# Optimization experiments

Measured on AMD Instinct MI355X. Metric: run time of the kernel, lower is better.

The kernel has to match this reference:

```python
import jax, jax.numpy as jnp
import numpy as np

N = 50000      # nodes
E = 800000     # edges (before self-loops)
F_IN = 128     # args.nsegment
H = 4          # args.nhead
C = 32         # args.dhidden
OUT = 64       # output_dim
G = 64         # number of graphs in batch
NEG = 0.2      # args.negslope (and GATv2 internal leaky-relu slope, PyG default 0.2)


def setup_inputs() -> dict:
    key = jax.random.key(0)
    ks = jax.random.split(key, 8)
    def w(k, i, o):
        return jax.random.normal(k, (i, o), jnp.float32) / np.sqrt(i)
    x = jax.random.normal(ks[0], (N, F_IN), jnp.float32)
    edge_index = jax.random.randint(ks[1], (2, E), 0, N, dtype=jnp.int32)
    batch = jnp.sort(jax.random.randint(ks[2], (N,), 0, G, dtype=jnp.int32))
    d = dict(x=x, edge_index=edge_index, batch=batch)
    # layer dims: (in_dim, heads, out_per_head, concat)
    dims = [(F_IN, H, C, True), (H * C, H, C, True), (H * C, 1, OUT, False)]
    for li, (fi, h, c, concat) in enumerate(dims):
        k1, k2, k3 = jax.random.split(ks[3 + li], 3)
        d[f"Wl{li}"] = w(k1, fi, h * c)
        d[f"Wr{li}"] = w(k2, fi, h * c)
        d[f"att{li}"] = jax.random.normal(k3, (h, c), jnp.float32) / np.sqrt(c)
        d[f"b{li}"] = jnp.zeros((h * c if concat else c,), jnp.float32)
    return d


def _gat_layer(x, src, tgt, Wl, Wr, att, b, concat):
    """GATv2Conv: e_ij = att . leaky_relu(Wl x_j + Wr x_i); softmax over edges into i;
    out_i = sum_j alpha_ij * (Wl x_j). src/tgt include self-loops."""
    n = x.shape[0]
    h, c = att.shape
    xl = (x @ Wl).reshape(n, h, c)                 # source transform [N,h,c]
    xr = (x @ Wr).reshape(n, h, c)                 # target transform [N,h,c]
    g = jax.nn.leaky_relu(xl[src] + xr[tgt], NEG)  # [Etot,h,c]
    score = jnp.einsum('ehc,hc->eh', g, att)       # [Etot,h]
    smax = jax.ops.segment_max(score, tgt, num_segments=n)
    ex = jnp.exp(score - smax[tgt])
    den = jax.ops.segment_sum(ex, tgt, num_segments=n)
    alpha = ex / den[tgt]                          # per-target softmax [Etot,h]
    out = jax.ops.segment_sum(xl[src] * alpha[:, :, None], tgt, num_segments=n)
    out = out.reshape(n, h * c) if concat else out.mean(axis=1)
    return out + b


def _forward(x, edge_index, batch, params):
    n = x.shape[0]
    loops = jnp.arange(n, dtype=edge_index.dtype)  # PyG add_self_loops=True
    src = jnp.concatenate([edge_index[0], loops])
    tgt = jnp.concatenate([edge_index[1], loops])
    for Wl, Wr, att, b, concat in params:
        x = _gat_layer(x, src, tgt, Wl, Wr, att, b, concat)
        x = jax.nn.leaky_relu(x, NEG)  # dropout p is identity in eval mode
    ssum = jax.ops.segment_sum(x, batch, num_segments=G)
    cnt = jax.ops.segment_sum(jnp.ones((n,), x.dtype), batch, num_segments=G)
    return ssum / jnp.maximum(cnt, 1.0)[:, None]   # global_mean_pool -> [G, OUT]


def reference(x, edge_index, batch, Wl0, Wr0, att0, b0, Wl1, Wr1, att1, b1, Wl2, Wr2, att2, b2):
    params = [(Wl0, Wr0, att0, b0, True),
              (Wl1, Wr1, att1, b1, True),
              (Wl2, Wr2, att2, b2, False)]
    return _forward(x, edge_index, batch, params)
```

## Files before the change

### kernel.cpp

```cpp
#include <hip/hip_runtime.h>
#include <hip/hip_fp16.h>
#include <math.h>

#define NEGSLOPE 0.2f

typedef _Float16 f16x8 __attribute__((ext_vector_type(8)));
typedef _Float16 f16x2 __attribute__((ext_vector_type(2)));
typedef float f32x4 __attribute__((ext_vector_type(4)));

__device__ __forceinline__ float lrelu(float x) { return x > 0.f ? x : NEGSLOPE * x; }

__device__ __forceinline__ float dot2acc(f16x2 a, f16x2 b, float c) {
#if __has_builtin(__builtin_amdgcn_fdot2)
    return __builtin_amdgcn_fdot2(a, b, c, false);
#else
    return c + (float)a[0] * (float)b[0] + (float)a[1] * (float)b[1];
#endif
}

__global__ __launch_bounds__(256) void k_prep(
        const float* W0, const float* W1, const float* W2,
        const float* W3, const float* W4, const float* W5,
        _Float16* D0, _Float16* D1, _Float16* D2,
        _Float16* D3, _Float16* D4, _Float16* D5,
        int* __restrict__ zbase, int nzero) {
    int b = blockIdx.x, t = threadIdx.x;
    if (b < 320) {
        const float* Ws[6] = {W0, W1, W2, W3, W4, W5};
        _Float16* Ds[6] = {D0, D1, D2, D3, D4, D5};
        int j = b * 256 + t;
        int m, jj, kout;
        if (j < 65536) { m = j >> 14; jj = j & 16383; kout = 128; }
        else           { m = 4 + ((j - 65536) >> 13); jj = (j - 65536) & 8191; kout = 64; }
        int col = jj >> 7, k = jj & 127;
        Ds[m][col * 128 + k] = (_Float16)Ws[m][k * kout + col];
    } else {
        int i = (b - 320) * 256 + t;
        if (i < nzero) zbase[i] = 0;
    }
}

__global__ void k_count(const int* __restrict__ tgt, int* __restrict__ deg,
                        int* __restrict__ rank, int e) {
    int i = blockIdx.x * 256 + threadIdx.x;
    if (i < e) rank[i] = atomicAdd(&deg[tgt[i]], 1);
}
__global__ __launch_bounds__(256) void k_scanA(const int* __restrict__ deg, int* __restrict__ rowptr,
                                               int* __restrict__ bsums, int* __restrict__ bhist, int n) {
    __shared__ int s[256];
    __shared__ int lh[64];
    int t = threadIdx.x;
    if (t < 64) lh[t] = 0;
    int base = blockIdx.x * 4096 + t * 16;
    int pre[16];
    int sum = 0;
    __syncthreads();
    for (int i = 0; i < 16; ++i) {
        int idx = base + i;
        int v = 0;
        if (idx < n) {
            v = deg[idx] + 1;
            atomicAdd(&lh[v < 63 ? v : 63], 1);
        }
        pre[i] = sum;
        sum += v;
    }
    s[t] = sum;
    __syncthreads();
    for (int off = 1; off < 256; off <<= 1) {
        int v = (t >= off) ? s[t - off] : 0;
        __syncthreads();
        s[t] += v;
        __syncthreads();
    }
    int tbase = s[t] - sum;
    for (int i = 0; i < 16; ++i) {
        int idx = base + i;
        if (idx < n) rowptr[idx] = tbase + pre[i];
    }
    if (t == 0) bsums[blockIdx.x] = s[255];
    if (t < 64) bhist[blockIdx.x * 64 + t] = lh[t];
}
__global__ __launch_bounds__(256) void k_scanC(int* __restrict__ rowptr, const int* __restrict__ bsums,
                                               int* __restrict__ edst, const int* __restrict__ deg,
                                               const int* __restrict__ bhist, int* __restrict__ perm,
                                               int nscan, int n) {
    __shared__ int pref[17];
    __shared__ int cur[64];
    __shared__ int bbase[64];
    int t = threadIdx.x;
    if (t == 0) {
        int run = 0;
        for (int k = 0; k < nscan; ++k) { pref[k] = run; run += bsums[k]; }
        pref[nscan] = run;
    }
    if (t < 64) {
        int part = 0, tot = 0;
        for (int sb = 0; sb < nscan; ++sb) {
            int v = bhist[sb * 64 + t];
            if (sb < (int)blockIdx.x) part += v;
            tot += v;
        }
        bbase[t] = tot;
        cur[t] = part;
    }
    __syncthreads();
    if (t == 0) {
        int run = 0;
        for (int k = 0; k < 64; ++k) { int v = bbase[k]; bbase[k] = run; run += v; }
    }
    __syncthreads();
    if (t < 64) cur[t] += bbase[t];
    __syncthreads();
    int myoff = pref[blockIdx.x];
    int base = blockIdx.x * 4096 + t * 16;
    for (int i = 0; i < 16; ++i) {
        int idx = base + i;
        if (idx < n) {
            int rp = rowptr[idx] + myoff;
            rowptr[idx] = rp;
            edst[rp] = idx;
            int d = deg[idx] + 1;
            int slot = atomicAdd(&cur[d < 63 ? d : 63], 1);
            perm[slot] = idx;
        }
    }
    if (blockIdx.x == gridDim.x - 1 && t == 0) rowptr[n] = pref[nscan];
}
__global__ void k_scatter(const int* __restrict__ src, const int* __restrict__ tgt,
                          const int* __restrict__ rank, const int* __restrict__ rowptr,
                          int* __restrict__ edst, int e) {
    int i = blockIdx.x * 256 + threadIdx.x;
    if (i < e) {
        int p = rowptr[tgt[i]] + 1 + rank[i];
        __builtin_nontemporal_store(src[i], &edst[p]);
    }
}

template<int KOUT, typename AT>
__global__ __launch_bounds__(256) void k_gemm_mfma(
        const AT* __restrict__ Ah,
        const _Float16* __restrict__ Wt0, const _Float16* __restrict__ Wt1,
        _Float16* __restrict__ out0, _Float16* __restrict__ out1, int n) {
    int wv = threadIdx.x >> 6, lane = threadIdx.x & 63;
    int m = lane & 15, q = lane >> 4;
    int row0 = blockIdx.x * 128 + wv * 32;
    int ra = row0 + m, rb = row0 + 16 + m;
    if (ra >= n) ra = n - 1;
    if (rb >= n) rb = n - 1;
    const AT* apa = Ah + (size_t)ra * 128 + q * 8;
    const AT* apb = Ah + (size_t)rb * 128 + q * 8;

    auto loadB = [](const AT* p) -> f16x8 {
        if constexpr (sizeof(AT) == 2) {
            return *(const f16x8*)p;
        } else {
            float4 a = *(const float4*)p, b = *(const float4*)(p + 4);
            f16x8 r;
            r[0] = (_Float16)a.x; r[1] = (_Float16)a.y; r[2] = (_Float16)a.z; r[3] = (_Float16)a.w;
            r[4] = (_Float16)b.x; r[5] = (_Float16)b.y; r[6] = (_Float16)b.z; r[7] = (_Float16)b.w;
            return r;
        }
    };

    const _Float16* Wp = Wt0;
    _Float16* outp = out0;
    if (KOUT == 128 && blockIdx.y) { Wp = Wt1; outp = out1; }

    f32x4 acc0[8] = {}, acc1[8] = {};
#pragma unroll
    for (int kt = 0; kt < 4; ++kt) {
        f16x8 wf[8];
#pragma unroll
        for (int ct = 0; ct < 8; ++ct) {
            const _Float16* W = (KOUT == 128) ? Wp : (ct < 4 ? Wt0 : Wt1);
            int col0 = (KOUT == 128) ? ct * 16 : (ct & 3) * 16;
            wf[ct] = *(const f16x8*)(W + (size_t)(col0 + m) * 128 + 32 * kt + 8 * q);
        }
        f16x8 bf0 = loadB(apa + 32 * kt);
        f16x8 bf1 = loadB(apb + 32 * kt);
#pragma unroll
        for (int ct = 0; ct < 8; ++ct) {
            acc0[ct] = __builtin_amdgcn_mfma_f32_16x16x32_f16(wf[ct], bf0, acc0[ct], 0, 0, 0);
            acc1[ct] = __builtin_amdgcn_mfma_f32_16x16x32_f16(wf[ct], bf1, acc1[ct], 0, 0, 0);
        }
    }
    int rowa = row0 + m, rowb = row0 + 16 + m;
#pragma unroll
    for (int ct = 0; ct < 8; ++ct) {
        _Float16* dst = (KOUT == 128) ? outp : (ct < 4 ? out0 : out1);
        int col = ((KOUT == 128) ? ct * 16 : (ct & 3) * 16) + q * 4;
        union { uint2 u; _Float16 h[4]; } pk;
        if (rowa < n) {
#pragma unroll
            for (int i = 0; i < 4; ++i) pk.h[i] = (_Float16)acc0[ct][i];
            *(uint2*)(dst + (size_t)rowa * KOUT + col) = pk.u;
        }
        if (rowb < n) {
#pragma unroll
            for (int i = 0; i < 4; ++i) pk.h[i] = (_Float16)acc1[ct][i];
            *(uint2*)(dst + (size_t)rowb * KOUT + col) = pk.u;
        }
    }
}

template<int H, int C, typename OutT>
__global__ __launch_bounds__(256) void k_agg(const _Float16* __restrict__ xl, const _Float16* __restrict__ xr,
                                             const float* __restrict__ att, const float* __restrict__ bias,
                                             const int* __restrict__ rowptr, const int* __restrict__ edst,
                                             const int* __restrict__ perm,
                                             OutT* __restrict__ yout, int n) {
    constexpr int F = H * C;
    constexpr int VEC = F / 16;
    constexpr int NH2 = VEC / 2;
    constexpr int L = C / VEC;
    int lane = threadIdx.x & 63;
    int wave = threadIdx.x >> 6;
    int s = lane & 15;
    int gid = blockIdx.x * 16 + wave * 4 + (lane >> 4);
    bool valid = gid < n;
    int node = valid ? perm[gid] : 0;
    int ch = s * VEC;

    union PkU { uint4 u4; uint2 u2v; f16x2 hh[4]; };

    f16x2 u2[NH2], av2[NH2];
    {
        PkU pk;
        if constexpr (NH2 == 4) pk.u4 = *(const uint4*)(xr + (size_t)node * F + ch);
        else pk.u2v = *(const uint2*)(xr + (size_t)node * F + ch);
#pragma unroll
        for (int j = 0; j < NH2; ++j) u2[j] = pk.hh[j];
    }
#pragma unroll
    for (int j = 0; j < NH2; ++j) {
        av2[j][0] = (_Float16)att[ch + 2 * j];
        av2[j][1] = (_Float16)att[ch + 2 * j + 1];
    }

    float acc[VEC];
#pragma unroll
    for (int j = 0; j < VEC; ++j) acc[j] = 0.f;
    int e0 = rowptr[node];
    int deg = valid ? (rowptr[node + 1] - e0) : 0;
    int maxdeg = deg;
    maxdeg = max(maxdeg, __shfl_xor(maxdeg, 16));
    maxdeg = max(maxdeg, __shfl_xor(maxdeg, 32));
    float ssum = 0.f;

    const _Float16 cneg = (_Float16)NEGSLOPE;
    auto loadrow = [&](int srcRow, PkU& pk) {
        const _Float16* p = xl + (size_t)srcRow * F + ch;
        if constexpr (NH2 == 4) pk.u4 = *(const uint4*)p;
        else pk.u2v = *(const uint2*)p;
    };
    auto process = [&](PkU& pk, bool live) {
        float sc = 0.f;
#pragma unroll
        for (int j = 0; j < NH2; ++j) {
            f16x2 t = pk.hh[j] + u2[j];
            f16x2 lr = __builtin_elementwise_max(t, t * cneg);
            sc = dot2acc(lr, av2[j], sc);
        }
#pragma unroll
        for (int off = 1; off < L; off <<= 1) sc += __shfl_xor(sc, off);
        float w = live ? __expf(sc) : 0.f;
        ssum += w;
#pragma unroll
        for (int j = 0; j < NH2; ++j) {
            acc[2 * j]     += w * (float)pk.hh[j][0];
            acc[2 * j + 1] += w * (float)pk.hh[j][1];
        }
    };

    for (int base = 0; base < maxdeg; base += 16) {
        int cnt = deg - base;
        if (cnt > 16) cnt = 16;
        int idxreg = (s < cnt) ? edst[e0 + base + s] : node;
        int mcnt = cnt;
        mcnt = max(mcnt, __shfl_xor(mcnt, 16));
        mcnt = max(mcnt, __shfl_xor(mcnt, 32));
        int gbase = lane & 48;
        int i = 0;
        for (; i + 4 <= mcnt; i += 4) {
            int s0 = __shfl(idxreg, gbase + i);
            int s1 = __shfl(idxreg, gbase + i + 1);
            int s2 = __shfl(idxreg, gbase + i + 2);
            int s3 = __shfl(idxreg, gbase + i + 3);
            PkU p0, p1, p2, p3;
            loadrow(s0, p0); loadrow(s1, p1); loadrow(s2, p2); loadrow(s3, p3);
            process(p0, i < cnt);
            process(p1, i + 1 < cnt);
            process(p2, i + 2 < cnt);
            process(p3, i + 3 < cnt);
        }
        for (; i < mcnt; ++i) {
            int s0 = __shfl(idxreg, gbase + i);
            PkU p0;
            loadrow(s0, p0);
            process(p0, i < cnt);
        }
    }
    if (valid) {
        float inv = 1.f / ssum;
        float o[VEC];
#pragma unroll
        for (int j = 0; j < VEC; ++j) o[j] = lrelu(acc[j] * inv + bias[ch + j]);
        if constexpr (sizeof(OutT) == 2) {
            _Float16* p = (_Float16*)yout + (size_t)node * F + ch;
            if constexpr (VEC == 8) {
                union { uint4 u; _Float16 h[8]; } pk;
#pragma unroll
                for (int j = 0; j < 8; ++j) pk.h[j] = (_Float16)o[j];
                *(uint4*)p = pk.u;
            } else {
                union { uint2 u; _Float16 h[4]; } pk;
#pragma unroll
                for (int j = 0; j < 4; ++j) pk.h[j] = (_Float16)o[j];
                *(uint2*)p = pk.u;
            }
        } else {
            float* p = (float*)yout + (size_t)node * F + ch;
            *(float4*)p = make_float4(o[0], o[1], o[2], o[3]);
            if constexpr (VEC == 8)
                *(float4*)(p + 4) = make_float4(o[4], o[5], o[6], o[7]);
        }
    }
}

__global__ __launch_bounds__(256) void k_pool_partial(const float* __restrict__ y,
        const int* __restrict__ batch, float* __restrict__ pacc, int n, int nchunk) {
    __shared__ float sdata[256];
    __shared__ int range[2];
    int g = blockIdx.x;
    int chunk = blockIdx.y;
    int t = threadIdx.x;
    if (t == 0) {
        int lo = 0, hi = n;
        while (lo < hi) { int mid = (lo + hi) >> 1; if (batch[mid] < g) lo = mid + 1; else hi = mid; }
        range[0] = lo;
        hi = n;
        while (lo < hi) { int mid = (lo + hi) >> 1; if (batch[mid] < g + 1) lo = mid + 1; else hi = mid; }
        range[1] = lo;
    }
    __syncthreads();
    int start = range[0], len = range[1] - range[0];
    int lo = start + (int)((long long)len * chunk / nchunk);
    int hi = start + (int)((long long)len * (chunk + 1) / nchunk);
    int ch = t & 63, sub = t >> 6;
    float acc = 0.f;
    for (int node = lo + sub; node < hi; node += 4)
        acc += y[(size_t)node * 64 + ch];
    sdata[t] = acc;
    __syncthreads();
    if (t < 128) sdata[t] += sdata[t + 128];
    __syncthreads();
    if (t < 64) atomicAdd(&pacc[g * 64 + t], sdata[t] + sdata[t + 64]);
}
__global__ void k_pool_final(const float* __restrict__ pacc, const int* __restrict__ batch,
                             float* __restrict__ out, int n) {
    __shared__ int cntS;
    int g = blockIdx.x, t = threadIdx.x;
    if (t == 0) {
        int lo = 0, hi = n;
        while (lo < hi) { int mid = (lo + hi) >> 1; if (batch[mid] < g) lo = mid + 1; else hi = mid; }
        int s = lo;
        hi = n;
        while (lo < hi) { int mid = (lo + hi) >> 1; if (batch[mid] < g + 1) lo = mid + 1; else hi = mid; }
        cntS = lo - s;
    }
    __syncthreads();
    out[g * 64 + t] = pacc[g * 64 + t] / fmaxf((float)cntS, 1.f);
}

extern "C" void kernel_launch(void* const* d_in, const int* in_sizes, int n_in,
                              void* d_out, int out_size, void* d_ws, size_t ws_size,
                              hipStream_t stream) {
    const float* x     = (const float*)d_in[0];
    const int*   ei    = (const int*)d_in[1];
    const int*   batch = (const int*)d_in[2];
    const float* Wl0 = (const float*)d_in[3];
    const float* Wr0 = (const float*)d_in[4];
    const float* att0 = (const float*)d_in[5];
    const float* b0  = (const float*)d_in[6];
    const float* Wl1 = (const float*)d_in[7];
    const float* Wr1 = (const float*)d_in[8];
    const float* att1 = (const float*)d_in[9];
    const float* b1  = (const float*)d_in[10];
    const float* Wl2 = (const float*)d_in[11];
    const float* Wr2 = (const float*)d_in[12];
    const float* att2 = (const float*)d_in[13];
    const float* b2  = (const float*)d_in[14];

    const int N = in_sizes[2];
    const int E = in_sizes[1] / 2;
    const int G = out_size / 64;
    const int* src = ei;
    const int* tgt = ei + E;

    size_t off = 0;
    auto take = [&](size_t bytes) {
        void* p = (char*)d_ws + off;
        off = (off + bytes + 255) & ~(size_t)255;
        return p;
    };
    _Float16* Ah   = (_Float16*)take((size_t)N * 128 * 2);
    _Float16* B    = (_Float16*)take((size_t)N * 128 * 2);
    _Float16* Cbh  = (_Float16*)take((size_t)N * 128 * 2);
    float* Cbf     = (float*)take((size_t)N * 64 * 4);
    _Float16* Wl0t = (_Float16*)take(128 * 128 * 2);
    _Float16* Wr0t = (_Float16*)take(128 * 128 * 2);
    _Float16* Wl1t = (_Float16*)take(128 * 128 * 2);
    _Float16* Wr1t = (_Float16*)take(128 * 128 * 2);
    _Float16* Wl2t = (_Float16*)take(64 * 128 * 2);
    _Float16* Wr2t = (_Float16*)take(64 * 128 * 2);
    int* rowptr = (int*)take((size_t)(N + 1) * 4);
    int* tmp    = (int*)take((size_t)N * 4);
    float* pacc = (float*)take((size_t)G * 64 * 4);
    int* bhist  = (int*)take(16 * 64 * 4);
    int* perm   = (int*)take((size_t)N * 4);
    int* rank   = (int*)take((size_t)E * 4);
    int* edst   = (int*)take((size_t)(E + N) * 4);
    int* bsums  = (int*)take(64 * 4);
    (void)ws_size; (void)n_in;

    const int TB = 256;
    int nblkE = (E + TB - 1) / TB;
    int nscan = (N + 4095) / 4096;

    int nzero = (int)(((char*)bhist) - (char*)tmp) / 4;
    int ZB = (nzero + TB - 1) / TB;
    k_prep<<<320 + ZB, TB, 0, stream>>>(
        Wl0, Wr0, Wl1, Wr1, Wl2, Wr2,
        Wl0t, Wr0t, Wl1t, Wr1t, Wl2t, Wr2t,
        tmp, nzero);

    k_count<<<nblkE, TB, 0, stream>>>(tgt, tmp, rank, E);
    k_scanA<<<nscan, TB, 0, stream>>>(tmp, rowptr, bsums, bhist, N);
    k_scanC<<<nscan, TB, 0, stream>>>(rowptr, bsums, edst, tmp, bhist, perm, nscan, N);
    k_scatter<<<nblkE, TB, 0, stream>>>(src, tgt, rank, rowptr, edst, E);

    int gemmBlocks = (N + 127) / 128;
    dim3 gemmGrid2(gemmBlocks, 2);
    dim3 gemmGrid1(gemmBlocks, 1);
    int aggBlocks = (N + 15) / 16;

    k_gemm_mfma<128, float><<<gemmGrid2, TB, 0, stream>>>(x, Wl0t, Wr0t, Ah, B, N);
    k_agg<4, 32, _Float16><<<aggBlocks, TB, 0, stream>>>(Ah, B, att0, b0, rowptr, edst, perm, Cbh, N);

    k_gemm_mfma<128, _Float16><<<gemmGrid2, TB, 0, stream>>>(Cbh, Wl1t, Wr1t, Ah, B, N);
    k_agg<4, 32, _Float16><<<aggBlocks, TB, 0, stream>>>(Ah, B, att1, b1, rowptr, edst, perm, Cbh, N);

    k_gemm_mfma<64, _Float16><<<gemmGrid1, TB, 0, stream>>>(Cbh, Wl2t, Wr2t, Ah, B, N);
    k_agg<1, 64, float><<<aggBlocks, TB, 0, stream>>>(Ah, B, att2, b2, rowptr, edst, perm, Cbf, N);

    dim3 poolGrid(G, 16);
    k_pool_partial<<<poolGrid, TB, 0, stream>>>(Cbf, batch, pacc, N, 16);
    k_pool_final<<<G, 64, 0, stream>>>(pacc, batch, (float*)d_out, N);
}
```

Baseline: 358.3 us.

## Co-schedule layer-0 GEMM halves with edge count and scatter kernels

Splits the layer-0 projection GEMM into its Wl and Wr halves and runs each as extra blocks inside the edge-count and edge-scatter kernels. The latency-bound atomic and scatter passes then overlap with MFMA compute, and one kernel launch goes away. The cost is heavier blocks sharing the grid with light ones, which may hurt occupancy and scheduling balance in those kernels.

```diff
diff --git a/kernel.cpp b/kernel.cpp
--- a/kernel.cpp
+++ b/kernel.cpp
@@ -40,10 +40,90 @@
     }
 }
 
-__global__ void k_count(const int* __restrict__ tgt, int* __restrict__ deg,
-                        int* __restrict__ rank, int e) {
-    int i = blockIdx.x * 256 + threadIdx.x;
-    if (i < e) rank[i] = atomicAdd(&deg[tgt[i]], 1);
+template<typename AT>
+__device__ __forceinline__ void gemm_pass128(int gblk, const AT* __restrict__ Ah,
+        const _Float16* __restrict__ Wp, _Float16* __restrict__ outp, int n) {
+    int wv = threadIdx.x >> 6, lane = threadIdx.x & 63;
+    int m = lane & 15, q = lane >> 4;
+    int row0 = gblk * 128 + wv * 32;
+    int ra = row0 + m, rb = row0 + 16 + m;
+    if (ra >= n) ra = n - 1;
+    if (rb >= n) rb = n - 1;
+    const AT* apa = Ah + (size_t)ra * 128 + q * 8;
+    const AT* apb = Ah + (size_t)rb * 128 + q * 8;
+
+    auto loadB = [](const AT* p) -> f16x8 {
+        if constexpr (sizeof(AT) == 2) {
+            return *(const f16x8*)p;
+        } else {
+            float4 a = *(const float4*)p, b = *(const float4*)(p + 4);
+            f16x8 r;
+            r[0] = (_Float16)a.x; r[1] = (_Float16)a.y; r[2] = (_Float16)a.z; r[3] = (_Float16)a.w;
+            r[4] = (_Float16)b.x; r[5] = (_Float16)b.y; r[6] = (_Float16)b.z; r[7] = (_Float16)b.w;
+            return r;
+        }
+    };
+
+    f32x4 acc0[8] = {}, acc1[8] = {};
+#pragma unroll
+    for (int kt = 0; kt < 4; ++kt) {
+        f16x8 wf[8];
+#pragma unroll
+        for (int ct = 0; ct < 8; ++ct)
+            wf[ct] = *(const f16x8*)(Wp + (size_t)(ct * 16 + m) * 128 + 32 * kt + 8 * q);
+        f16x8 bf0 = loadB(apa + 32 * kt);
+        f16x8 bf1 = loadB(apb + 32 * kt);
+#pragma unroll
+        for (int ct = 0; ct < 8; ++ct) {
+            acc0[ct] = __builtin_amdgcn_mfma_f32_16x16x32_f16(wf[ct], bf0, acc0[ct], 0, 0, 0);
+            acc1[ct] = __builtin_amdgcn_mfma_f32_16x16x32_f16(wf[ct], bf1, acc1[ct], 0, 0, 0);
+        }
+    }
+    int rowa = row0 + m, rowb = row0 + 16 + m;
+#pragma unroll
+    for (int ct = 0; ct < 8; ++ct) {
+        int col = ct * 16 + q * 4;
+        union { uint2 u; _Float16 h[4]; } pk;
+        if (rowa < n) {
+#pragma unroll
+            for (int i = 0; i < 4; ++i) pk.h[i] = (_Float16)acc0[ct][i];
+            *(uint2*)(outp + (size_t)rowa * 128 + col) = pk.u;
+        }
+        if (rowb < n) {
+#pragma unroll
+            for (int i = 0; i < 4; ++i) pk.h[i] = (_Float16)acc1[ct][i];
+            *(uint2*)(outp + (size_t)rowb * 128 + col) = pk.u;
+        }
+    }
+}
+
+__global__ __launch_bounds__(256) void k_count_gemm(
+        const int* __restrict__ tgt, int* __restrict__ deg, int* __restrict__ rank,
+        int e, int nblkE,
+        const float* __restrict__ x, const _Float16* __restrict__ Wl0t,
+        _Float16* __restrict__ Ah, int n) {
+    if ((int)blockIdx.x < nblkE) {
+        int i = blockIdx.x * 256 + threadIdx.x;
+        if (i < e) rank[i] = atomicAdd(&deg[tgt[i]], 1);
+    } else {
+        gemm_pass128<float>(blockIdx.x - nblkE, x, Wl0t, Ah, n);
+    }
+}
+__global__ __launch_bounds__(256) void k_scatter_gemm(
+        const int* __restrict__ src, const int* __restrict__ tgt,
+        const int* __restrict__ rank, const int* __restrict__ rowptr,
+        int* __restrict__ edst, int e, int nblkE,
+        const float* __restrict__ x, const _Float16* __restrict__ Wr0t,
+        _Float16* __restrict__ B, int n) {
+    if ((int)blockIdx.x < nblkE) {
+        int i = blockIdx.x * 256 + threadIdx.x;
+        if (i < e) {
+            int p = rowptr[tgt[i]] + 1 + rank[i];
+            __builtin_nontemporal_store(src[i], &edst[p]);
+        }
+    } else {
+        gemm_pass128<float>(blockIdx.x - nblkE, x, Wr0t, B, n);
+    }
 }
 __global__ __launch_bounds__(256) void k_scanA(const int* __restrict__ deg, int* __restrict__ rowptr,
                                                int* __restrict__ bsums, int* __restrict__ bhist, int n) {
@@ -126,15 +206,6 @@
         }
     }
     if (blockIdx.x == gridDim.x - 1 && t == 0) rowptr[n] = pref[nscan];
-}
-__global__ void k_scatter(const int* __restrict__ src, const int* __restrict__ tgt,
-                          const int* __restrict__ rank, const int* __restrict__ rowptr,
-                          int* __restrict__ edst, int e) {
-    int i = blockIdx.x * 256 + threadIdx.x;
-    if (i < e) {
-        int p = rowptr[tgt[i]] + 1 + rank[i];
-        __builtin_nontemporal_store(src[i], &edst[p]);
-    }
 }
 
 template<int KOUT, typename AT>
@@ -427,6 +498,7 @@
     const int TB = 256;
     int nblkE = (E + TB - 1) / TB;
     int nscan = (N + 4095) / 4096;
+    int gemmBlocks = (N + 127) / 128;
 
     int nzero = (int)(((char*)bhist) - (char*)tmp) / 4;
     int ZB = (nzero + TB - 1) / TB;
@@ -435,17 +507,17 @@
         Wl0t, Wr0t, Wl1t, Wr1t, Wl2t, Wr2t,
         tmp, nzero);
 
-    k_count<<<nblkE, TB, 0, stream>>>(tgt, tmp, rank, E);
+    k_count_gemm<<<nblkE + gemmBlocks, TB, 0, stream>>>(
+        tgt, tmp, rank, E, nblkE, x, Wl0t, Ah, N);
     k_scanA<<<nscan, TB, 0, stream>>>(tmp, rowptr, bsums, bhist, N);
     k_scanC<<<nscan, TB, 0, stream>>>(rowptr, bsums, edst, tmp, bhist, perm, nscan, N);
-    k_scatter<<<nblkE, TB, 0, stream>>>(src, tgt, rank, rowptr, edst, E);
-
-    int gemmBlocks = (N + 127) / 128;
+    k_scatter_gemm<<<nblkE + gemmBlocks, TB, 0, stream>>>(
+        src, tgt, rank, rowptr, edst, E, nblkE, x, Wr0t, B, N);
+
     dim3 gemmGrid2(gemmBlocks, 2);
     dim3 gemmGrid1(gemmBlocks, 1);
     int aggBlocks = (N + 15) / 16;
 
-    k_gemm_mfma<128, float><<<gemmGrid2, TB, 0, stream>>>(x, Wl0t, Wr0t, Ah, B, N);
     k_agg<4, 32, _Float16><<<aggBlocks, TB, 0, stream>>>(Ah, B, att0, b0, rowptr, edst, perm, Cbh, N);
 
     k_gemm_mfma<128, _Float16><<<gemmGrid2, TB, 0, stream>>>(Cbh, Wl1t, Wr1t, Ah, B, N);
```

After: 365.8 us. 1.02x slower.
